# Kernel optimization log

Hardware: AMD Instinct MI355X
Metric: run time of the kernel (lower is better)

## Reference

```python
import jax, jax.numpy as jnp
import numpy as np

N_HEADS = 16

def setup_inputs() -> dict:
    key = jax.random.key(0)
    k1, k2, k3, k4 = jax.random.split(key, 4)
    B, N, E = 4, 2048, 1024
    x = jax.random.normal(k1, (B, N, E), dtype=jnp.float32)
    s = 1.0 / np.sqrt(E)
    Wq = jax.random.normal(k2, (E, E), dtype=jnp.float32) * s
    Wk = jax.random.normal(k3, (E, E), dtype=jnp.float32) * s
    Wv = jax.random.normal(k4, (E, E), dtype=jnp.float32) * s
    return {"x": x, "Wq": Wq, "Wk": Wk, "Wv": Wv}

def reference(x, Wq, Wk, Wv):
    # first_block=False -> PositionalEncoding is identity: encoded_vectors = x
    B, N, E = x.shape
    H = N_HEADS
    D = E // H
    norm = np.sqrt(D).astype(np.float32)
    # torch nn.Linear(bias=False): y = x @ W.T
    q = (x @ Wq.T).reshape(B, N, H, D).transpose(0, 2, 1, 3)  # [B,H,N,D]
    k = (x @ Wk.T).reshape(B, N, H, D).transpose(0, 2, 1, 3)
    v = (x @ Wv.T).reshape(B, N, H, D).transpose(0, 2, 1, 3)
    scores = jnp.einsum('bhnd,bhmd->bhnm', q, k) / norm  # [B,H,N,N]
    attn = jax.nn.softmax(scores, axis=-1)
    # original einsum 'stuu, stuv -> stuv': diagonal of attn scales values
    diag = jnp.diagonal(attn, axis1=-2, axis2=-1)  # [B,H,N]
    av = diag[..., None] * v  # [B,H,N,D]
    av = av.transpose(0, 2, 1, 3).reshape(B, N, E)
    return (av, x)
```

## Files before the change

kernel.cpp:

```cpp
#include <hip/hip_runtime.h>
#include <hip/hip_bf16.h>
#include <stdint.h>

typedef __attribute__((ext_vector_type(8))) short short8;
typedef __attribute__((ext_vector_type(4))) float f32x4;

#define BATCH 4
#define SEQ   2048
#define EMB   1024
#define HEADS 16
#define DHEAD 64
#define MROWS (BATCH * SEQ)
#define NW    (EMB * EMB)

#define QSCALE 0.18033688011112042f

__device__ inline unsigned short f2bf(float f) {
    unsigned int u = __float_as_uint(f);
    unsigned int r = (u + 0x7fffu + ((u >> 16) & 1u)) >> 16;
    return (unsigned short)r;
}

__device__ __forceinline__ void gl_lds16(const short* g, short* l) {
    __builtin_amdgcn_global_load_lds(
        (const __attribute__((address_space(1))) void*)g,
        (__attribute__((address_space(3))) void*)l, 16, 0, 0);
}

template <int N>
__device__ __forceinline__ void waitvm() {
    asm volatile("s_waitcnt vmcnt(%0)" :: "n"(N) : "memory");
}

__global__ __launch_bounds__(256) void pack_all(const float* __restrict__ x,
                                                const float* __restrict__ wq,
                                                const float* __restrict__ wk,
                                                const float* __restrict__ wv,
                                                unsigned short* __restrict__ xb,
                                                unsigned short* __restrict__ wb,
                                                float* __restrict__ pass) {
    const int i = (blockIdx.x * 256 + threadIdx.x) * 8;
    const float* src;
    unsigned short* dst;
    bool isx = i < MROWS * EMB;
    if (isx) {
        src = x + i;
        dst = xb + i;
    } else {
        const int j = i - MROWS * EMB;
        src = (j < NW) ? wq + j : (j < 2 * NW) ? wk + (j - NW) : wv + (j - 2 * NW);
        dst = wb + j;
    }
    const float4* s = reinterpret_cast<const float4*>(src);
    float4 f0 = s[0];
    float4 f1 = s[1];
    union { unsigned short u[8]; short8 v; } o;
    o.u[0] = f2bf(f0.x); o.u[1] = f2bf(f0.y); o.u[2] = f2bf(f0.z); o.u[3] = f2bf(f0.w);
    o.u[4] = f2bf(f1.x); o.u[5] = f2bf(f1.y); o.u[6] = f2bf(f1.z); o.u[7] = f2bf(f1.w);
    *reinterpret_cast<short8*>(dst) = o.v;
    if (isx) {
        float4* p = reinterpret_cast<float4*>(pass + i);
        p[0] = f0;
        p[1] = f1;
    }
}

template <int MODE>
__global__ __launch_bounds__(512, 2) void gemm8(const short* __restrict__ A,
                                                const short* __restrict__ Bm,
                                                unsigned short* __restrict__ Cb,
                                                float* __restrict__ out,
                                                const float* __restrict__ dgp) {
    constexpr int K = EMB;
    constexpr int NT = K / 32;
    constexpr int BN = (MODE == 0) ? 256 : 128;
    constexpr int NF = BN / 64;
    constexpr int BUFSTRIDE = 8192 + BN * 32;
    constexpr int VW = 2 + BN / 128;

    __shared__ short Ks[3 * BUFSTRIDE];

    const int t = threadIdx.x;
    const int lane = t & 63;
    const int w = t >> 6;
    const int wr = w >> 2;
    const int wc = w & 3;
    const int rl = lane & 15;
    const int pg = (lane >> 4) ^ (lane & 3);
    const int m0 = blockIdx.x * 256;
    const int n0 = blockIdx.y * BN;

    const int sr = t >> 2;
    const int sg = (t & 3) ^ (sr & 3);
    const int soff = sr * K + sg * 8;
    const short* gA0 = A + (size_t)(m0)*K + soff;
    const short* gA1 = A + (size_t)(m0 + 128) * K + soff;
    const short* gB0 = Bm + (size_t)(n0)*K + soff;
    const short* gB1 = Bm + (size_t)(n0 + 128) * K + soff;
    short* ldsw = Ks + w * 512;

#define STAGE8(kk, bb)                                               \
    {                                                                \
        const int _k = (kk)*32;                                      \
        short* _l = ldsw + (bb)*BUFSTRIDE;                           \
        gl_lds16(gA0 + _k, _l);                                      \
        gl_lds16(gA1 + _k, _l + 4096);                               \
        gl_lds16(gB0 + _k, _l + 8192);                               \
        if (MODE == 0) gl_lds16(gB1 + _k, _l + 12288);               \
    }

    f32x4 acc[8][NF] = {};

    STAGE8(0, 0);
    STAGE8(1, 1);
    waitvm<VW>();
    __builtin_amdgcn_s_barrier();

    int cur = 0;
    for (int kt = 0; kt < NT; ++kt) {
        const int pf = kt + 2;
        if (pf < NT) {
            int nb = cur + 2; if (nb >= 3) nb -= 3;
            STAGE8(pf, nb);
        }

        const short* bufp = Ks + cur * BUFSTRIDE;
        short8 av[8], bv[NF];
#pragma unroll
        for (int i = 0; i < 8; i++)
            av[i] = *(const short8*)&bufp[wr * 4096 + i * 512 + rl * 32 + pg * 8];
#pragma unroll
        for (int j = 0; j < NF; j++) {
            const int brow = (MODE == 0) ? ((wc & 1) * 64 + j * 16 + rl)
                                         : (wc * 32 + j * 16 + rl);
            const int bh = (MODE == 0) ? (wc >> 1) : 0;
            bv[j] = *(const short8*)&bufp[8192 + bh * 4096 + brow * 32 + pg * 8];
        }

        __builtin_amdgcn_s_setprio(1);
#pragma unroll
        for (int i = 0; i < 8; i++)
#pragma unroll
            for (int j = 0; j < NF; j++)
                acc[i][j] = __builtin_amdgcn_mfma_f32_16x16x32_bf16(av[i], bv[j], acc[i][j], 0, 0, 0);
        __builtin_amdgcn_s_setprio(0);

        if (kt < NT - 2) waitvm<VW>();
        else             waitvm<0>();
        __builtin_amdgcn_s_barrier();

        cur += 1; if (cur == 3) cur = 0;
    }
#undef STAGE8

    const int gr_base = m0 + wr * 128 + (lane >> 4) * 4;
    const int gc_base = n0 + wc * (BN / 4) + rl;
#pragma unroll
    for (int i = 0; i < 8; i++) {
#pragma unroll
        for (int j = 0; j < NF; j++) {
            const int col = gc_base + j * 16;
#pragma unroll
            for (int r = 0; r < 4; r++) {
                const int grow = gr_base + i * 16 + r;
                const int bb = grow >> 11;
                const int nn = grow & 2047;
                if (MODE == 0) {
                    const int sel = col >> 10;
                    const int cc = col & 1023;
                    const int hh = cc >> 6;
                    const int dd = cc & 63;
                    const float sc = sel ? 1.0f : QSCALE;
                    Cb[(((size_t)((sel << 6) + (bb << 4) + hh) * SEQ + nn) << 6) + dd] =
                        f2bf(acc[i][j][r] * sc);
                } else {
                    const int hh = col >> 6;
                    const float d = dgp[((bb << 4) + hh) * SEQ + nn];
                    out[(size_t)grow * EMB + col] = acc[i][j][r] * d;
                }
            }
        }
    }
}

__global__ __launch_bounds__(256, 2) void diag_kernel(const short* __restrict__ Qh,
                                                      const short* __restrict__ Kh,
                                                      float* __restrict__ dgp) {
    const int n = blockIdx.x;
    const int bh = (n & 7) | ((n >> 6) << 3);
    const int qt = (n >> 3) & 7;
    const int t = threadIdx.x;
    const int lane = t & 63;
    const int w = t >> 6;
    const int rl = lane & 15;
    const int g = lane >> 4;
    const int kq = g * 8;

    const short* Kbh = Kh + (size_t)bh * SEQ * DHEAD;
    const short* Qbh = Qh + (size_t)bh * SEQ * DHEAD;

    const int qbase = qt * 256 + w * 64;
    short8 a0[4], a1[4];
#pragma unroll
    for (int i = 0; i < 4; i++) {
        const int qrow = qbase + i * 16 + rl;
        a0[i] = *(const short8*)(Qbh + qrow * DHEAD + kq);
        a1[i] = *(const short8*)(Qbh + qrow * DHEAD + kq + 32);
    }

    float sdiag[4];
    const int rr = rl - g * 4;
#pragma unroll
    for (int i = 0; i < 4; i++) {
        const int krow = qbase + i * 16 + rl;
        const short8 b0d = *(const short8*)(Kbh + krow * DHEAD + kq);
        const short8 b1d = *(const short8*)(Kbh + krow * DHEAD + kq + 32);
        f32x4 cd = {};
        cd = __builtin_amdgcn_mfma_f32_16x16x32_bf16(a0[i], b0d, cd, 0, 0, 0);
        cd = __builtin_amdgcn_mfma_f32_16x16x32_bf16(a1[i], b1d, cd, 0, 0, 0);
        sdiag[i] = (rr >= 0 && rr < 4) ? cd[rr] : 0.f;
    }

    const short* kp = Kbh + rl * DHEAD + kq;

#define LOADS(s, b0v, b1v)                                      \
    {                                                           \
        const short* _p = kp + (s) * (16 * DHEAD);              \
        b0v = *(const short8*)_p;                               \
        b1v = *(const short8*)(_p + 32);                        \
    }
#define COMP(b0v, b1v)                                                              \
    {                                                                               \
        _Pragma("unroll") for (int i = 0; i < 4; i++) {                             \
            f32x4 c;                                                               \
            c = __builtin_amdgcn_mfma_f32_16x16x32_bf16(a0[i], b0v, f32x4{}, 0, 0, 0); \
            c = __builtin_amdgcn_mfma_f32_16x16x32_bf16(a1[i], b1v, c, 0, 0, 0);    \
            _Pragma("unroll") for (int r = 0; r < 4; ++r)                           \
                ssum[i][r] += __builtin_amdgcn_exp2f(c[r]);                         \
        }                                                                           \
    }

    float ssum[4][4] = {};

    short8 eb0, eb1, ob0, ob1;
    LOADS(0, eb0, eb1);
    LOADS(1, ob0, ob1);
    for (int s = 0; s < 126; s += 2) {
        short8 n0, n1, m0, m1;
        LOADS(s + 2, n0, n1);
        LOADS(s + 3, m0, m1);
        COMP(eb0, eb1);
        COMP(ob0, ob1);
        eb0 = n0; eb1 = n1;
        ob0 = m0; ob1 = m1;
    }
    COMP(eb0, eb1);
    COMP(ob0, ob1);
#undef LOADS
#undef COMP

#pragma unroll
    for (int i = 0; i < 4; i++)
#pragma unroll
        for (int r = 0; r < 4; r++) {
            float v = ssum[i][r];
            v += __shfl_xor(v, 1);
            v += __shfl_xor(v, 2);
            v += __shfl_xor(v, 4);
            v += __shfl_xor(v, 8);
            ssum[i][r] = v;
        }

    if (rr >= 0 && rr < 4) {
#pragma unroll
        for (int i = 0; i < 4; i++) {
            const float dg = __builtin_amdgcn_exp2f(sdiag[i]) / ssum[i][rr];
            dgp[bh * SEQ + qbase + i * 16 + rl] = dg;
        }
    }
}

extern "C" void kernel_launch(void* const* d_in, const int* in_sizes, int n_in,
                              void* d_out, int out_size, void* d_ws, size_t ws_size,
                              hipStream_t stream) {
    const float* x  = (const float*)d_in[0];
    const float* Wq = (const float*)d_in[1];
    const float* Wk = (const float*)d_in[2];
    const float* Wv = (const float*)d_in[3];
    float* out = (float*)d_out;
    char* ws = (char*)d_ws;

    const size_t xb_off  = 0;
    const size_t wq_off  = xb_off + (size_t)MROWS * EMB * 2;
    const size_t wk_off  = wq_off + (size_t)NW * 2;
    const size_t wv_off  = wk_off + (size_t)NW * 2;
    const size_t q_off   = wv_off + (size_t)NW * 2;
    const size_t k_off   = q_off + (size_t)MROWS * EMB * 2;
    const size_t dg_off  = k_off + (size_t)MROWS * EMB * 2;

    short* xb  = (short*)(ws + xb_off);
    short* wqb = (short*)(ws + wq_off);
    short* wvb = (short*)(ws + wv_off);
    short* Qh  = (short*)(ws + q_off);
    short* Kh  = (short*)(ws + k_off);
    float* dgp = (float*)(ws + dg_off);

    const int npack = (MROWS * EMB + 3 * NW) / 2048;

    pack_all<<<npack, 256, 0, stream>>>(x, Wq, Wk, Wv,
                                        (unsigned short*)xb, (unsigned short*)wqb,
                                        out + (size_t)MROWS * EMB);

    gemm8<0><<<dim3(MROWS / 256, 2048 / 256), 512, 0, stream>>>(
        xb, wqb, (unsigned short*)Qh, nullptr, nullptr);

    diag_kernel<<<512, 256, 0, stream>>>(Qh, Kh, dgp);

    gemm8<1><<<dim3(MROWS / 256, EMB / 128), 512, 0, stream>>>(
        xb, wvb, nullptr, out, dgp);
}
```

Measured before the change: 150.4 us.

## Split diag softmax-denominator over key chunks and stage K through LDS

The diagonal-softmax kernel now splits the key dimension into four chunks, launching four times as many blocks. Each block writes a partial row-sum, and a new combine kernel adds the partials and divides by the diagonal numerator. K tiles are streamed into swizzled LDS buffers with a three-deep async global-to-LDS pipeline instead of direct register loads. This is meant to improve occupancy and latency hiding in the exp-sum pass, at the cost of an extra launch and partial-sum traffic.

```diff
diff --git a/kernel.cpp b/kernel.cpp
--- a/kernel.cpp
+++ b/kernel.cpp
@@ -183,12 +183,16 @@
     }
 }
 
-__global__ __launch_bounds__(256, 2) void diag_kernel(const short* __restrict__ Qh,
+__global__ __launch_bounds__(256, 5) void diag_kernel(const short* __restrict__ Qh,
                                                       const short* __restrict__ Kh,
-                                                      float* __restrict__ dgp) {
+                                                      float* __restrict__ num,
+                                                      float* __restrict__ pp) {
     const int n = blockIdx.x;
-    const int bh = (n & 7) | ((n >> 6) << 3);
+    const int bh = (n & 7) | ((n >> 8) << 3);
     const int qt = (n >> 3) & 7;
+    const int ks = (n >> 6) & 3;
+    __shared__ short Ksd[4 * 3 * 1024];
+
     const int t = threadIdx.x;
     const int lane = t & 63;
     const int w = t >> 6;
@@ -208,56 +212,77 @@
         a1[i] = *(const short8*)(Qbh + qrow * DHEAD + kq + 32);
     }
 
-    float sdiag[4];
     const int rr = rl - g * 4;
-#pragma unroll
-    for (int i = 0; i < 4; i++) {
-        const int krow = qbase + i * 16 + rl;
-        const short8 b0d = *(const short8*)(Kbh + krow * DHEAD + kq);
-        const short8 b1d = *(const short8*)(Kbh + krow * DHEAD + kq + 32);
-        f32x4 cd = {};
-        cd = __builtin_amdgcn_mfma_f32_16x16x32_bf16(a0[i], b0d, cd, 0, 0, 0);
-        cd = __builtin_amdgcn_mfma_f32_16x16x32_bf16(a1[i], b1d, cd, 0, 0, 0);
-        sdiag[i] = (rr >= 0 && rr < 4) ? cd[rr] : 0.f;
-    }
-
-    const short* kp = Kbh + rl * DHEAD + kq;
-
-#define LOADS(s, b0v, b1v)                                      \
-    {                                                           \
-        const short* _p = kp + (s) * (16 * DHEAD);              \
-        b0v = *(const short8*)_p;                               \
-        b1v = *(const short8*)(_p + 32);                        \
-    }
-#define COMP(b0v, b1v)                                                              \
-    {                                                                               \
-        _Pragma("unroll") for (int i = 0; i < 4; i++) {                             \
-            f32x4 c;                                                               \
-            c = __builtin_amdgcn_mfma_f32_16x16x32_bf16(a0[i], b0v, f32x4{}, 0, 0, 0); \
-            c = __builtin_amdgcn_mfma_f32_16x16x32_bf16(a1[i], b1v, c, 0, 0, 0);    \
-            _Pragma("unroll") for (int r = 0; r < 4; ++r)                           \
-                ssum[i][r] += __builtin_amdgcn_exp2f(c[r]);                         \
-        }                                                                           \
-    }
+
+    if (ks == 0) {
+        float sdiag[4];
+#pragma unroll
+        for (int i = 0; i < 4; i++) {
+            const int krow = qbase + i * 16 + rl;
+            const short8 b0d = *(const short8*)(Kbh + krow * DHEAD + kq);
+            const short8 b1d = *(const short8*)(Kbh + krow * DHEAD + kq + 32);
+            f32x4 cd = {};
+            cd = __builtin_amdgcn_mfma_f32_16x16x32_bf16(a0[i], b0d, cd, 0, 0, 0);
+            cd = __builtin_amdgcn_mfma_f32_16x16x32_bf16(a1[i], b1d, cd, 0, 0, 0);
+            sdiag[i] = (rr >= 0 && rr < 4) ? cd[rr] : 0.f;
+        }
+        if (rr >= 0 && rr < 4) {
+#pragma unroll
+            for (int i = 0; i < 4; i++)
+                num[bh * SEQ + qbase + i * 16 + rl] =
+                    __builtin_amdgcn_exp2f(sdiag[i]);
+        }
+    }
+
+    const int sr8 = lane >> 3;
+    const int sg = (lane & 7) ^ sr8;
+    const short* gkb = Kbh + (size_t)ks * 512 * DHEAD + sr8 * DHEAD + sg * 8;
+    short* ldsw = Ksd + w * 3072;
+
+#define DSTAGE(s, b)                                         \
+    {                                                        \
+        const short* _src = gkb + (s) * (16 * DHEAD);        \
+        gl_lds16(_src, ldsw + (b)*1024);                     \
+        gl_lds16(_src + 8 * DHEAD, ldsw + (b)*1024 + 512);   \
+    }
+
+    const int rb0 = (g ^ (rl & 7)) * 8;
+    const int rb1 = ((g + 4) ^ (rl & 7)) * 8;
 
     float ssum[4][4] = {};
 
-    short8 eb0, eb1, ob0, ob1;
-    LOADS(0, eb0, eb1);
-    LOADS(1, ob0, ob1);
-    for (int s = 0; s < 126; s += 2) {
-        short8 n0, n1, m0, m1;
-        LOADS(s + 2, n0, n1);
-        LOADS(s + 3, m0, m1);
-        COMP(eb0, eb1);
-        COMP(ob0, ob1);
-        eb0 = n0; eb1 = n1;
-        ob0 = m0; ob1 = m1;
-    }
-    COMP(eb0, eb1);
-    COMP(ob0, ob1);
-#undef LOADS
-#undef COMP
+    waitvm<0>();
+    DSTAGE(0, 0);
+    DSTAGE(1, 1);
+
+    int bufi = 0;
+    for (int s = 0; s < 32; ++s) {
+        if (s < 30) {
+            int nb = bufi + 2; if (nb >= 3) nb -= 3;
+            DSTAGE(s + 2, nb);
+            waitvm<4>();
+        } else if (s == 30) {
+            waitvm<2>();
+        } else {
+            waitvm<0>();
+        }
+
+        const short* rrow = ldsw + bufi * 1024 + rl * 64;
+        const short8 b0 = *(const short8*)(rrow + rb0);
+        const short8 b1 = *(const short8*)(rrow + rb1);
+#pragma unroll
+        for (int i = 0; i < 4; i++) {
+            f32x4 c;
+            c = __builtin_amdgcn_mfma_f32_16x16x32_bf16(a0[i], b0, f32x4{}, 0, 0, 0);
+            c = __builtin_amdgcn_mfma_f32_16x16x32_bf16(a1[i], b1, c, 0, 0, 0);
+#pragma unroll
+            for (int r = 0; r < 4; ++r)
+                ssum[i][r] += __builtin_amdgcn_exp2f(c[r]);
+        }
+
+        bufi += 1; if (bufi == 3) bufi = 0;
+    }
+#undef DSTAGE
 
 #pragma unroll
     for (int i = 0; i < 4; i++)
@@ -273,11 +298,18 @@
 
     if (rr >= 0 && rr < 4) {
 #pragma unroll
-        for (int i = 0; i < 4; i++) {
-            const float dg = __builtin_amdgcn_exp2f(sdiag[i]) / ssum[i][rr];
-            dgp[bh * SEQ + qbase + i * 16 + rl] = dg;
-        }
-    }
+        for (int i = 0; i < 4; i++)
+            pp[(ks * 64 + bh) * SEQ + qbase + i * 16 + rl] = ssum[i][rr];
+    }
+}
+
+__global__ __launch_bounds__(256) void combine_dgp(const float* __restrict__ num,
+                                                   const float* __restrict__ pp,
+                                                   float* __restrict__ dgp) {
+    const int i = blockIdx.x * 256 + threadIdx.x;
+    const float s = pp[i] + pp[i + 64 * SEQ * 1] + pp[i + 64 * SEQ * 2] +
+                    pp[i + 64 * SEQ * 3];
+    dgp[i] = num[i] / s;
 }
 
 extern "C" void kernel_launch(void* const* d_in, const int* in_sizes, int n_in,
@@ -296,13 +328,17 @@
     const size_t wv_off  = wk_off + (size_t)NW * 2;
     const size_t q_off   = wv_off + (size_t)NW * 2;
     const size_t k_off   = q_off + (size_t)MROWS * EMB * 2;
-    const size_t dg_off  = k_off + (size_t)MROWS * EMB * 2;
+    const size_t num_off = k_off + (size_t)MROWS * EMB * 2;
+    const size_t pp_off  = num_off + (size_t)64 * SEQ * 4;
+    const size_t dg_off  = pp_off + (size_t)4 * 64 * SEQ * 4;
 
     short* xb  = (short*)(ws + xb_off);
     short* wqb = (short*)(ws + wq_off);
     short* wvb = (short*)(ws + wv_off);
     short* Qh  = (short*)(ws + q_off);
     short* Kh  = (short*)(ws + k_off);
+    float* num = (float*)(ws + num_off);
+    float* pp  = (float*)(ws + pp_off);
     float* dgp = (float*)(ws + dg_off);
 
     const int npack = (MROWS * EMB + 3 * NW) / 2048;
@@ -314,7 +350,9 @@
     gemm8<0><<<dim3(MROWS / 256, 2048 / 256), 512, 0, stream>>>(
         xb, wqb, (unsigned short*)Qh, nullptr, nullptr);
 
-    diag_kernel<<<512, 256, 0, stream>>>(Qh, Kh, dgp);
+    diag_kernel<<<2048, 256, 0, stream>>>(Qh, Kh, num, pp);
+
+    combine_dgp<<<64 * SEQ / 256, 256, 0, stream>>>(num, pp, dgp);
 
     gemm8<1><<<dim3(MROWS / 256, EMB / 128), 512, 0, stream>>>(
         xb, wvb, nullptr, out, dgp);
```

Measured after the change: 137.5 us. -8.6%, faster.

## Stage K tiles in swizzled LDS and use 32x32 MFMA in diag kernel

Applied to the files above, without the earlier changes.

The softmax-denominator kernel now uses 512-thread blocks with 8 waves of 32 query rows each. K tiles are double-buffered through XOR-swizzled shared memory so all waves share one global load of each tile. The inner product switches from 16x16x32 to 32x32x16 MFMA with 16-element accumulators. This cuts redundant global K reads and raises MFMA efficiency, at the cost of extra block barriers, LDS traffic, and a more intricate lane mapping for the diagonal gather.

```diff
diff --git a/kernel.cpp b/kernel.cpp
--- a/kernel.cpp
+++ b/kernel.cpp
@@ -4,6 +4,7 @@
 
 typedef __attribute__((ext_vector_type(8))) short short8;
 typedef __attribute__((ext_vector_type(4))) float f32x4;
+typedef __attribute__((ext_vector_type(16))) float f32x16;
 
 #define BATCH 4
 #define SEQ   2048
@@ -183,99 +184,130 @@
     }
 }
 
-__global__ __launch_bounds__(256, 2) void diag_kernel(const short* __restrict__ Qh,
+__global__ __launch_bounds__(512, 4) void diag_kernel(const short* __restrict__ Qh,
                                                       const short* __restrict__ Kh,
                                                       float* __restrict__ dgp) {
     const int n = blockIdx.x;
     const int bh = (n & 7) | ((n >> 6) << 3);
     const int qt = (n >> 3) & 7;
+    __shared__ short Ksd[2 * 8192];
+
     const int t = threadIdx.x;
     const int lane = t & 63;
     const int w = t >> 6;
-    const int rl = lane & 15;
-    const int g = lane >> 4;
-    const int kq = g * 8;
+    const int qbase = qt * 256 + w * 32;
 
     const short* Kbh = Kh + (size_t)bh * SEQ * DHEAD;
     const short* Qbh = Qh + (size_t)bh * SEQ * DHEAD;
 
-    const int qbase = qt * 256 + w * 64;
-    short8 a0[4], a1[4];
-#pragma unroll
-    for (int i = 0; i < 4; i++) {
-        const int qrow = qbase + i * 16 + rl;
-        a0[i] = *(const short8*)(Qbh + qrow * DHEAD + kq);
-        a1[i] = *(const short8*)(Qbh + qrow * DHEAD + kq + 32);
-    }
-
-    float sdiag[4];
-    const int rr = rl - g * 4;
-#pragma unroll
-    for (int i = 0; i < 4; i++) {
-        const int krow = qbase + i * 16 + rl;
-        const short8 b0d = *(const short8*)(Kbh + krow * DHEAD + kq);
-        const short8 b1d = *(const short8*)(Kbh + krow * DHEAD + kq + 32);
+    const int rl16 = lane & 15;
+    const int g16 = lane >> 4;
+    const int kq = g16 * 8;
+    const int rr = rl16 - g16 * 4;
+    float sdiag[2];
+#pragma unroll
+    for (int i = 0; i < 2; i++) {
+        const int row = qbase + i * 16 + rl16;
+        const short8 a0d = *(const short8*)(Qbh + row * DHEAD + kq);
+        const short8 a1d = *(const short8*)(Qbh + row * DHEAD + kq + 32);
+        const short8 b0d = *(const short8*)(Kbh + row * DHEAD + kq);
+        const short8 b1d = *(const short8*)(Kbh + row * DHEAD + kq + 32);
         f32x4 cd = {};
-        cd = __builtin_amdgcn_mfma_f32_16x16x32_bf16(a0[i], b0d, cd, 0, 0, 0);
-        cd = __builtin_amdgcn_mfma_f32_16x16x32_bf16(a1[i], b1d, cd, 0, 0, 0);
+        cd = __builtin_amdgcn_mfma_f32_16x16x32_bf16(a0d, b0d, cd, 0, 0, 0);
+        cd = __builtin_amdgcn_mfma_f32_16x16x32_bf16(a1d, b1d, cd, 0, 0, 0);
         sdiag[i] = (rr >= 0 && rr < 4) ? cd[rr] : 0.f;
     }
 
-    const short* kp = Kbh + rl * DHEAD + kq;
-
-#define LOADS(s, b0v, b1v)                                      \
-    {                                                           \
-        const short* _p = kp + (s) * (16 * DHEAD);              \
-        b0v = *(const short8*)_p;                               \
-        b1v = *(const short8*)(_p + 32);                        \
-    }
-#define COMP(b0v, b1v)                                                              \
-    {                                                                               \
-        _Pragma("unroll") for (int i = 0; i < 4; i++) {                             \
-            f32x4 c;                                                               \
-            c = __builtin_amdgcn_mfma_f32_16x16x32_bf16(a0[i], b0v, f32x4{}, 0, 0, 0); \
-            c = __builtin_amdgcn_mfma_f32_16x16x32_bf16(a1[i], b1v, c, 0, 0, 0);    \
-            _Pragma("unroll") for (int r = 0; r < 4; ++r)                           \
-                ssum[i][r] += __builtin_amdgcn_exp2f(c[r]);                         \
-        }                                                                           \
-    }
-
-    float ssum[4][4] = {};
-
-    short8 eb0, eb1, ob0, ob1;
-    LOADS(0, eb0, eb1);
-    LOADS(1, ob0, ob1);
-    for (int s = 0; s < 126; s += 2) {
-        short8 n0, n1, m0, m1;
-        LOADS(s + 2, n0, n1);
-        LOADS(s + 3, m0, m1);
-        COMP(eb0, eb1);
-        COMP(ob0, ob1);
-        eb0 = n0; eb1 = n1;
-        ob0 = m0; ob1 = m1;
-    }
-    COMP(eb0, eb1);
-    COMP(ob0, ob1);
-#undef LOADS
-#undef COMP
-
-#pragma unroll
-    for (int i = 0; i < 4; i++)
-#pragma unroll
-        for (int r = 0; r < 4; r++) {
-            float v = ssum[i][r];
-            v += __shfl_xor(v, 1);
-            v += __shfl_xor(v, 2);
-            v += __shfl_xor(v, 4);
-            v += __shfl_xor(v, 8);
-            ssum[i][r] = v;
-        }
-
-    if (rr >= 0 && rr < 4) {
-#pragma unroll
-        for (int i = 0; i < 4; i++) {
-            const float dg = __builtin_amdgcn_exp2f(sdiag[i]) / ssum[i][rr];
-            dgp[bh * SEQ + qbase + i * 16 + rl] = dg;
+    const int r32 = lane & 31;
+    const int h = lane >> 5;
+    short8 aq[4];
+    {
+        const short* qp = Qbh + (qbase + r32) * DHEAD + h * 8;
+#pragma unroll
+        for (int m = 0; m < 4; m++)
+            aq[m] = *(const short8*)(qp + m * 16);
+    }
+
+    const int sr = t >> 3;
+    const int c0 = t & 7;
+    const int cs = (c0 ^ (sr & 7)) * 8;
+
+    *(short8*)&Ksd[sr * 64 + cs]          = *(const short8*)&Kbh[sr * DHEAD + c0 * 8];
+    *(short8*)&Ksd[(sr + 64) * 64 + cs]   = *(const short8*)&Kbh[(sr + 64) * DHEAD + c0 * 8];
+    __syncthreads();
+
+    int voff[4];
+#pragma unroll
+    for (int m = 0; m < 4; m++)
+        voff[m] = r32 * 64 + (((2 * m + h) ^ (r32 & 7)) * 8);
+
+    f32x16 ssum = {};
+
+#define DCOMP(BUFSEL, SUBBASE)                                                     \
+    {                                                                              \
+        _Pragma("unroll") for (int sub = 0; sub < 4; ++sub) {                      \
+            const int base = (BUFSEL)*8192 + sub * 2048;                           \
+            const short8 b0 = *(const short8*)&Ksd[base + voff[0]];                \
+            const short8 b1 = *(const short8*)&Ksd[base + voff[1]];                \
+            const short8 b2 = *(const short8*)&Ksd[base + voff[2]];                \
+            const short8 b3 = *(const short8*)&Ksd[base + voff[3]];                \
+            f32x16 c = __builtin_amdgcn_mfma_f32_32x32x16_bf16(aq[0], b0, (f32x16){}, 0, 0, 0); \
+            c = __builtin_amdgcn_mfma_f32_32x32x16_bf16(aq[1], b1, c, 0, 0, 0);    \
+            c = __builtin_amdgcn_mfma_f32_32x32x16_bf16(aq[2], b2, c, 0, 0, 0);    \
+            c = __builtin_amdgcn_mfma_f32_32x32x16_bf16(aq[3], b3, c, 0, 0, 0);    \
+            _Pragma("unroll") for (int e = 0; e < 16; ++e)                         \
+                ssum[e] += __builtin_amdgcn_exp2f(c[e]);                           \
+        }                                                                          \
+    }
+
+    for (int kt = 0; kt < 16; kt += 2) {
+        short8 pa0, pa1;
+        {
+            const short* src = Kbh + (kt + 1) * 8192;
+            pa0 = *(const short8*)&src[sr * DHEAD + c0 * 8];
+            pa1 = *(const short8*)&src[(sr + 64) * DHEAD + c0 * 8];
+        }
+        DCOMP(0, kt);
+        __syncthreads();
+        *(short8*)&Ksd[8192 + sr * 64 + cs]        = pa0;
+        *(short8*)&Ksd[8192 + (sr + 64) * 64 + cs] = pa1;
+        __syncthreads();
+
+        short8 pb0, pb1;
+        const bool more = (kt + 2) < 16;
+        if (more) {
+            const short* src = Kbh + (kt + 2) * 8192;
+            pb0 = *(const short8*)&src[sr * DHEAD + c0 * 8];
+            pb1 = *(const short8*)&src[(sr + 64) * DHEAD + c0 * 8];
+        }
+        DCOMP(1, kt + 1);
+        if (more) {
+            __syncthreads();
+            *(short8*)&Ksd[sr * 64 + cs]        = pb0;
+            *(short8*)&Ksd[(sr + 64) * 64 + cs] = pb1;
+            __syncthreads();
+        }
+    }
+#undef DCOMP
+
+#pragma unroll
+    for (int e = 0; e < 16; ++e) {
+        float v = ssum[e];
+        v += __shfl_xor(v, 1);
+        v += __shfl_xor(v, 2);
+        v += __shfl_xor(v, 4);
+        v += __shfl_xor(v, 8);
+        v += __shfl_xor(v, 16);
+        ssum[e] = v;
+    }
+
+#pragma unroll
+    for (int r = 0; r < 16; ++r) {
+        const int srcl = 40 * ((r >> 2) & 1) + 20 * h + (r & 3);
+        const float nm = __shfl(sdiag[r >> 3], srcl);
+        if (r32 == r) {
+            const int row = (r & 3) + 8 * (r >> 2) + 4 * h;
+            dgp[bh * SEQ + qbase + row] = __builtin_amdgcn_exp2f(nm) / ssum[r];
         }
     }
 }
@@ -314,7 +346,7 @@
     gemm8<0><<<dim3(MROWS / 256, 2048 / 256), 512, 0, stream>>>(
         xb, wqb, (unsigned short*)Qh, nullptr, nullptr);
 
-    diag_kernel<<<512, 256, 0, stream>>>(Qh, Kh, dgp);
+    diag_kernel<<<512, 512, 0, stream>>>(Qh, Kh, dgp);
 
     gemm8<1><<<dim3(MROWS / 256, EMB / 128), 512, 0, stream>>>(
         xb, wvb, nullptr, out, dgp);
```

Measured after the change: 138.6 us. 1.08x faster.
